# Kernel optimization log

Hardware: AMD Instinct MI355X
Metric: run time of the kernel (lower is better)

## Reference

```python
import jax, jax.numpy as jnp
import numpy as np

N_NODES = 40000
N_EDGES = 640000
IN_FEATS = 256
EDGE_FEATS = 64
OUT_FEATS = 128
NUM_HEADS = 8
D = OUT_FEATS // NUM_HEADS  # 16


def setup_inputs() -> dict:
    key = jax.random.key(0)
    ks = jax.random.split(key, 9)
    node_feats = jax.random.normal(ks[0], (N_NODES, IN_FEATS), dtype=jnp.float32)
    edge_feats = jax.random.normal(ks[1], (N_EDGES, EDGE_FEATS), dtype=jnp.float32)
    src = jax.random.randint(ks[2], (N_EDGES,), 0, N_NODES, dtype=jnp.int32)
    dst = jax.random.randint(ks[3], (N_EDGES,), 0, N_NODES, dtype=jnp.int32)
    # learned parameters (xavier-ish scale)
    node_w = jax.random.normal(ks[4], (OUT_FEATS, IN_FEATS), dtype=jnp.float32) * (2.0 / (IN_FEATS + OUT_FEATS)) ** 0.5
    node_b = jnp.zeros((OUT_FEATS,), dtype=jnp.float32)
    edge_w = jax.random.normal(ks[5], (OUT_FEATS, EDGE_FEATS), dtype=jnp.float32) * (2.0 / (EDGE_FEATS + OUT_FEATS)) ** 0.5
    edge_b = jnp.zeros((OUT_FEATS,), dtype=jnp.float32)
    attn = jax.random.normal(ks[6], (1, NUM_HEADS, 3 * D), dtype=jnp.float32) * 0.1
    return {"node_feats": node_feats, "edge_feats": edge_feats, "src": src, "dst": dst,
            "node_w": node_w, "node_b": node_b, "edge_w": edge_w, "edge_b": edge_b, "attn": attn}


def reference(node_feats, edge_feats, src, dst, node_w, node_b, edge_w, edge_b, attn):
    N = node_feats.shape[0]
    # Node / edge projections -> [N,H,D], [E,H,D]
    Wh = (node_feats @ node_w.T + node_b).reshape(-1, NUM_HEADS, D)
    We = (edge_feats @ edge_w.T + edge_b).reshape(-1, NUM_HEADS, D)
    # Split attn into src/dst/edge parts: attn is [1,H,3D]
    a = attn[0]  # [H,3D]
    a_src, a_dst, a_e = a[:, :D], a[:, D:2 * D], a[:, 2 * D:]
    # Per-node partial scores [N,H], then gather per edge; edge part [E,H]
    s_src = jnp.einsum('nhd,hd->nh', Wh, a_src)
    s_dst = jnp.einsum('nhd,hd->nh', Wh, a_dst)
    s_e = jnp.einsum('ehd,hd->eh', We, a_e)
    e = s_src[src] + s_dst[dst] + s_e  # [E,H]
    e = jax.nn.leaky_relu(e, negative_slope=0.2)
    # Edge softmax over incoming edges of each dst node
    m = jax.ops.segment_max(e, dst, num_segments=N)          # [N,H]
    ex = jnp.exp(e - m[dst])                                  # [E,H]
    z = jax.ops.segment_sum(ex, dst, num_segments=N)          # [N,H]
    alpha = ex / z[dst]                                       # [E,H]
    # Weighted scatter-sum aggregation of source features
    msg = alpha[:, :, None] * Wh[src]                         # [E,H,D]
    h = jax.ops.segment_sum(msg, dst, num_segments=N)         # [N,H,D]
    return h.reshape(N, NUM_HEADS * D)
```

## Files before the change

### kernel.cpp

```cpp
#include <hip/hip_runtime.h>
#include <hip/hip_fp16.h>
#include <stdint.h>
#include <stddef.h>

#define N_NODES   40000
#define N_EDGES   640000
#define IN_FEATS  256
#define EDGE_FEATS 64
#define OUT_FEATS 128
#define NUM_HEADS 8
#define HD        16

typedef __attribute__((ext_vector_type(8))) short  short8;
typedef __attribute__((ext_vector_type(4))) float  floatx4;

__device__ inline short f2bf(float f) {
  union { float f; uint32_t u; } v; v.f = f;
  uint32_t r = v.u + 0x7fffu + ((v.u >> 16) & 1u);
  return (short)(r >> 16);
}

__device__ inline short8 cvt8(float4 lo, float4 hi) {
  short8 r;
  r[0] = f2bf(lo.x); r[1] = f2bf(lo.y); r[2] = f2bf(lo.z); r[3] = f2bf(lo.w);
  r[4] = f2bf(hi.x); r[5] = f2bf(hi.y); r[6] = f2bf(hi.z); r[7] = f2bf(hi.w);
  return r;
}

__device__ inline float bflo(uint32_t w) {
  union { uint32_t u; float f; } v; v.u = w << 16; return v.f;
}
__device__ inline float bfhi(uint32_t w) {
  union { uint32_t u; float f; } v; v.u = w & 0xffff0000u; return v.f;
}

__global__ __launch_bounds__(512) void prep_hist_kernel(
    const float* __restrict__ edge_w, const float* __restrict__ edge_b,
    const float* __restrict__ attn, const float* __restrict__ node_w,
    const int* __restrict__ dst,
    float* __restrict__ Wfold, float* __restrict__ bfold,
    uint32_t* __restrict__ Wbf, int* __restrict__ deg) {
  int tid = threadIdx.x;
  if (blockIdx.x == 0) {
    int h = tid >> 6, k = tid & 63;
    float s = 0.f;
    #pragma unroll
    for (int d = 0; d < HD; d++)
      s += edge_w[(h * HD + d) * EDGE_FEATS + k] * attn[h * 48 + 32 + d];
    Wfold[h * EDGE_FEATS + k] = s;
    if (k == 0) {
      float b = 0.f;
      #pragma unroll
      for (int d = 0; d < HD; d++)
        b += edge_b[h * HD + d] * attn[h * 48 + 32 + d];
      bfold[h] = b;
    }
    const float2* W2 = (const float2*)node_w;
    #pragma unroll
    for (int j = 0; j < 32; j++) {
      int p = j * 512 + tid;
      float2 f = W2[p];
      Wbf[p] = (uint32_t)(uint16_t)f2bf(f.x) |
               ((uint32_t)(uint16_t)f2bf(f.y) << 16);
    }
  } else {
    int e = (blockIdx.x - 1) * 512 + tid;
    atomicAdd(&deg[dst[e]], 1);
  }
}

__global__ __launch_bounds__(256) void wh_gemm(
    const float* __restrict__ A,
    const uint32_t* __restrict__ Wbf,
    const float* __restrict__ bias,
    uint32_t* __restrict__ Whp) {
  int wave = (blockIdx.x * blockDim.x + threadIdx.x) >> 6;
  int lane = threadIdx.x & 63;
  int m0 = wave * 16;
  if (m0 >= N_NODES) return;
  int row = lane & 15, quad = lane >> 4;

  floatx4 acc[8];
  #pragma unroll
  for (int nt = 0; nt < 8; nt++) acc[nt] = (floatx4)(0.f);

  const float4* A4 = (const float4*)A;
  const uint4*  W4 = (const uint4*)Wbf;
  int a_base = ((m0 + row) * IN_FEATS + quad * 8) >> 2;

  #pragma unroll
  for (int s = 0; s < 8; s++) {
    float4 alo = A4[a_base + s * 8];
    float4 ahi = A4[a_base + s * 8 + 1];
    short8 af = cvt8(alo, ahi);
    #pragma unroll
    for (int nt = 0; nt < 8; nt++) {
      int fo = (nt * 16 + row) * IN_FEATS + s * 32 + quad * 8;
      uint4 u = W4[fo >> 3];
      short8 bf = *(short8*)&u;
      acc[nt] = __builtin_amdgcn_mfma_f32_16x16x32_bf16(af, bf, acc[nt], 0, 0, 0);
    }
  }
  #pragma unroll
  for (int nt = 0; nt < 4; nt++) {
    float blo_ = bias[nt * 16 + row];
    float bhi_ = bias[64 + nt * 16 + row];
    #pragma unroll
    for (int r = 0; r < 4; r++) {
      int m = m0 + quad * 4 + r;
      float lo = acc[nt][r] + blo_;
      float hi = acc[nt + 4][r] + bhi_;
      uint32_t d = (uint32_t)(uint16_t)f2bf(lo) |
                   ((uint32_t)(uint16_t)f2bf(hi) << 16);
      Whp[m * 64 + nt * 16 + row] = d;
    }
  }
}

__global__ __launch_bounds__(256) void ssd_kernel(
    const uint32_t* __restrict__ Whp, const float* __restrict__ attn,
    float* __restrict__ s_src, float* __restrict__ s_dst) {
  int t = blockIdx.x * 256 + threadIdx.x;
  int n = t >> 2, hp = t & 3;
  const uint4* p = (const uint4*)(Whp + n * 64 + hp * 16);
  const float* as_lo = attn + hp * 48;
  const float* ad_lo = attn + hp * 48 + 16;
  const float* as_hi = attn + (hp + 4) * 48;
  const float* ad_hi = attn + (hp + 4) * 48 + 16;
  float ss_lo = 0.f, sd_lo = 0.f, ss_hi = 0.f, sd_hi = 0.f;
  #pragma unroll
  for (int q = 0; q < 4; q++) {
    uint4 u = p[q];
    uint32_t ws[4] = {u.x, u.y, u.z, u.w};
    #pragma unroll
    for (int k = 0; k < 4; k++) {
      int d = q * 4 + k;
      float lo = bflo(ws[k]), hi = bfhi(ws[k]);
      ss_lo += lo * as_lo[d]; sd_lo += lo * ad_lo[d];
      ss_hi += hi * as_hi[d]; sd_hi += hi * ad_hi[d];
    }
  }
  s_src[n * 8 + hp]     = ss_lo;
  s_src[n * 8 + hp + 4] = ss_hi;
  s_dst[n * 8 + hp]     = sd_lo;
  s_dst[n * 8 + hp + 4] = sd_hi;
}

__global__ __launch_bounds__(1024) void scan_kernel(
    const int* __restrict__ deg, int* __restrict__ rs, int* __restrict__ cursor) {
  __shared__ int wsum[16];
  __shared__ int carry;
  int tid = threadIdx.x;
  int lane = tid & 63, w = tid >> 6;
  if (tid == 0) carry = 0;
  __syncthreads();
  for (int chunk = 0; chunk < 40; chunk++) {
    int i = chunk * 1024 + tid;
    int v = (i < N_NODES) ? deg[i] : 0;
    int x = v;
    #pragma unroll
    for (int off = 1; off < 64; off <<= 1) {
      int y = __shfl_up(x, off, 64);
      if (lane >= off) x += y;
    }
    if (lane == 63) wsum[w] = x;
    __syncthreads();
    int p = carry, tot = 0;
    #pragma unroll
    for (int j = 0; j < 16; j++) {
      int s = wsum[j];
      if (j < w) p += s;
      tot += s;
    }
    int excl = p + x - v;
    if (i < N_NODES) { rs[i] = excl; cursor[i] = excl; }
    __syncthreads();
    if (tid == 0) carry += tot;
  }
  __syncthreads();
  if (tid == 0) rs[N_NODES] = carry;
}

__global__ __launch_bounds__(256) void edge_kernel(
    const float* __restrict__ edge_feats, const int* __restrict__ src,
    const int* __restrict__ dst, const float* __restrict__ Wfold,
    const float* __restrict__ bfold, const float* __restrict__ s_src,
    const float* __restrict__ s_dst, uint4* __restrict__ lg16) {
  int e = blockIdx.x * 256 + threadIdx.x;
  int s = src[e], d = dst[e];
  const float4* ss4 = (const float4*)(s_src + (size_t)s * 8);
  const float4* sd4 = (const float4*)(s_dst + (size_t)d * 8);
  float4 sa = ss4[0], sb = ss4[1];
  float4 da = sd4[0], db = sd4[1];

  float acc[8];
  #pragma unroll
  for (int h = 0; h < 8; h++) acc[h] = bfold[h];
  const float4* ef4 = (const float4*)(edge_feats + (size_t)e * EDGE_FEATS);
  #pragma unroll
  for (int k4 = 0; k4 < 16; k4++) {
    float4 f = ef4[k4];
    #pragma unroll
    for (int h = 0; h < 8; h++) {
      const float* wr = Wfold + h * EDGE_FEATS + k4 * 4;
      acc[h] += f.x * wr[0] + f.y * wr[1] + f.z * wr[2] + f.w * wr[3];
    }
  }
  float v[8];
  v[0] = acc[0] + sa.x + da.x; v[1] = acc[1] + sa.y + da.y;
  v[2] = acc[2] + sa.z + da.z; v[3] = acc[3] + sa.w + da.w;
  v[4] = acc[4] + sb.x + db.x; v[5] = acc[5] + sb.y + db.y;
  v[6] = acc[6] + sb.z + db.z; v[7] = acc[7] + sb.w + db.w;
  #pragma unroll
  for (int h = 0; h < 8; h++) v[h] = v[h] > 0.f ? v[h] : 0.2f * v[h];

  uint32_t pk[4];
  #pragma unroll
  for (int j = 0; j < 4; j++) {
    uint32_t lo = __half_as_ushort(__float2half_rn(v[2 * j]));
    uint32_t hi = __half_as_ushort(__float2half_rn(v[2 * j + 1]));
    pk[j] = lo | (hi << 16);
  }
  lg16[e] = make_uint4(pk[0], pk[1], pk[2], pk[3]);
}

__global__ __launch_bounds__(256) void scatter_kernel(
    const int* __restrict__ src, const int* __restrict__ dst,
    int* __restrict__ cursor, int2* __restrict__ csr8) {
  int e = blockIdx.x * 256 + threadIdx.x;
  int d = dst[e];
  int s = src[e];
  int pos = atomicAdd(&cursor[d], 1);
  csr8[pos] = make_int2(e, s);
}

__global__ __launch_bounds__(256) void aggregate_kernel(
    const int* __restrict__ rs, const int2* __restrict__ csr8,
    const uint4* __restrict__ lg16, const uint32_t* __restrict__ Whp,
    float* __restrict__ out) {
  int node = blockIdx.x * 4 + (threadIdx.x >> 6);
  int lane = threadIdx.x & 63;
  int h1 = lane >> 4;
  int start = rs[node], end = rs[node + 1];
  uint32_t sh = (h1 & 1) * 16;
  bool hi_pair = (h1 & 2) != 0;

  float z1 = 0.f, z2 = 0.f, a1 = 0.f, a2 = 0.f;

  #define STEP(g, wv)                                                  \
    {                                                                  \
      uint32_t c1 = hi_pair ? (g).y : (g).x;                           \
      uint32_t c2 = hi_pair ? (g).w : (g).z;                           \
      float l1 = __half2float(__ushort_as_half((uint16_t)(c1 >> sh))); \
      float l2 = __half2float(__ushort_as_half((uint16_t)(c2 >> sh))); \
      float e1 = __expf(l1), e2 = __expf(l2);                          \
      z1 += e1; z2 += e2;                                              \
      a1 += e1 * bflo(wv); a2 += e2 * bfhi(wv);                        \
    }

  int i = start;
  for (; i + 3 < end; i += 4) {
    int2 r0 = csr8[i], r1 = csr8[i + 1], r2 = csr8[i + 2], r3 = csr8[i + 3];
    uint4 g0 = lg16[r0.x], g1 = lg16[r1.x], g2 = lg16[r2.x], g3 = lg16[r3.x];
    uint32_t w0 = Whp[(size_t)r0.y * 64 + lane];
    uint32_t w1 = Whp[(size_t)r1.y * 64 + lane];
    uint32_t w2 = Whp[(size_t)r2.y * 64 + lane];
    uint32_t w3 = Whp[(size_t)r3.y * 64 + lane];
    STEP(g0, w0); STEP(g1, w1); STEP(g2, w2); STEP(g3, w3);
  }
  for (; i < end; i++) {
    int2 r0 = csr8[i];
    uint4 g0 = lg16[r0.x];
    uint32_t w0 = Whp[(size_t)r0.y * 64 + lane];
    STEP(g0, w0);
  }
  #undef STEP

  float o1 = (end > start) ? a1 / z1 : 0.f;
  float o2 = (end > start) ? a2 / z2 : 0.f;
  out[(size_t)node * OUT_FEATS + lane] = o1;
  out[(size_t)node * OUT_FEATS + 64 + lane] = o2;
}

extern "C" void kernel_launch(void* const* d_in, const int* in_sizes, int n_in,
                              void* d_out, int out_size, void* d_ws, size_t ws_size,
                              hipStream_t stream) {
  const float* node_feats = (const float*)d_in[0];
  const float* edge_feats = (const float*)d_in[1];
  const int*   src        = (const int*)d_in[2];
  const int*   dst        = (const int*)d_in[3];
  const float* node_w     = (const float*)d_in[4];
  const float* node_b     = (const float*)d_in[5];
  const float* edge_w     = (const float*)d_in[6];
  const float* edge_b     = (const float*)d_in[7];
  const float* attn       = (const float*)d_in[8];
  float* out = (float*)d_out;

  char* ws = (char*)d_ws;
  size_t off = 0;
  auto alloc = [&](size_t bytes) {
    void* p = ws + off;
    off += (bytes + 255) & ~(size_t)255;
    return p;
  };
  uint32_t* Whp      = (uint32_t*)alloc((size_t)N_NODES * 64 * 4);
  float*    s_src    = (float*)alloc((size_t)N_NODES * NUM_HEADS * 4);
  float*    s_dst    = (float*)alloc((size_t)N_NODES * NUM_HEADS * 4);
  uint4*    lg16     = (uint4*)alloc((size_t)N_EDGES * 16);
  int2*     csr8     = (int2*)alloc((size_t)N_EDGES * 8);
  int*      deg      = (int*)alloc((size_t)N_NODES * 4);
  int*      rs       = (int*)alloc((size_t)(N_NODES + 1) * 4);
  int*      cursor   = (int*)alloc((size_t)N_NODES * 4);
  float*    Wfold    = (float*)alloc(NUM_HEADS * EDGE_FEATS * 4);
  float*    bfold    = (float*)alloc(NUM_HEADS * 4);
  uint32_t* Wbf      = (uint32_t*)alloc((size_t)OUT_FEATS * IN_FEATS * 2);

  hipMemsetAsync(deg, 0, (size_t)N_NODES * 4, stream);

  prep_hist_kernel<<<1 + N_EDGES / 512, 512, 0, stream>>>(
      edge_w, edge_b, attn, node_w, dst, Wfold, bfold, Wbf, deg);
  wh_gemm<<<N_NODES / 16 / 4, 256, 0, stream>>>(node_feats, Wbf, node_b, Whp);
  ssd_kernel<<<N_NODES * 4 / 256, 256, 0, stream>>>(Whp, attn, s_src, s_dst);
  scan_kernel<<<1, 1024, 0, stream>>>(deg, rs, cursor);
  edge_kernel<<<N_EDGES / 256, 256, 0, stream>>>(edge_feats, src, dst, Wfold,
                                                 bfold, s_src, s_dst, lg16);
  scatter_kernel<<<N_EDGES / 256, 256, 0, stream>>>(src, dst, cursor, csr8);
  aggregate_kernel<<<N_NODES / 4, 256, 0, stream>>>(rs, csr8, lg16, Whp, out);
}
```

Before: 471.9 us.

## Split each node's edges across two waves and halve scan iterations

```diff
diff --git a/kernel.cpp b/kernel.cpp
--- a/kernel.cpp
+++ b/kernel.cpp
@@ -154,9 +154,11 @@
   int lane = tid & 63, w = tid >> 6;
   if (tid == 0) carry = 0;
   __syncthreads();
-  for (int chunk = 0; chunk < 40; chunk++) {
-    int i = chunk * 1024 + tid;
-    int v = (i < N_NODES) ? deg[i] : 0;
+  const int2* deg2 = (const int2*)deg;
+  for (int chunk = 0; chunk < 20; chunk++) {
+    int i2 = chunk * 1024 + tid;
+    int2 dv = (i2 < N_NODES / 2) ? deg2[i2] : make_int2(0, 0);
+    int v = dv.x + dv.y;
     int x = v;
     #pragma unroll
     for (int off = 1; off < 64; off <<= 1) {
@@ -173,7 +175,10 @@
       tot += s;
     }
     int excl = p + x - v;
-    if (i < N_NODES) { rs[i] = excl; cursor[i] = excl; }
+    if (i2 < N_NODES / 2) {
+      rs[2 * i2]     = excl;      cursor[2 * i2]     = excl;
+      rs[2 * i2 + 1] = excl + dv.x; cursor[2 * i2 + 1] = excl + dv.x;
+    }
     __syncthreads();
     if (tid == 0) carry += tot;
   }
@@ -238,10 +243,18 @@
     const int* __restrict__ rs, const int2* __restrict__ csr8,
     const uint4* __restrict__ lg16, const uint32_t* __restrict__ Whp,
     float* __restrict__ out) {
-  int node = blockIdx.x * 4 + (threadIdx.x >> 6);
+  __shared__ float red[2][4][64];
+  int w = threadIdx.x >> 6;
   int lane = threadIdx.x & 63;
+  int nib = w >> 1;
+  int sub = w & 1;
+  int node = blockIdx.x * 2 + nib;
   int h1 = lane >> 4;
   int start = rs[node], end = rs[node + 1];
+  int cnt = end - start;
+  int half = (cnt + 1) >> 1;
+  int s0 = start + sub * half;
+  int e0 = min(end, s0 + half);
   uint32_t sh = (h1 & 1) * 16;
   bool hi_pair = (h1 & 2) != 0;
 
@@ -258,17 +271,32 @@
       a1 += e1 * bflo(wv); a2 += e2 * bfhi(wv);                        \
     }
 
-  int i = start;
-  for (; i + 3 < end; i += 4) {
-    int2 r0 = csr8[i], r1 = csr8[i + 1], r2 = csr8[i + 2], r3 = csr8[i + 3];
-    uint4 g0 = lg16[r0.x], g1 = lg16[r1.x], g2 = lg16[r2.x], g3 = lg16[r3.x];
-    uint32_t w0 = Whp[(size_t)r0.y * 64 + lane];
-    uint32_t w1 = Whp[(size_t)r1.y * 64 + lane];
-    uint32_t w2 = Whp[(size_t)r2.y * 64 + lane];
-    uint32_t w3 = Whp[(size_t)r3.y * 64 + lane];
-    STEP(g0, w0); STEP(g1, w1); STEP(g2, w2); STEP(g3, w3);
-  }
-  for (; i < end; i++) {
+  int i = s0;
+  for (; i + 7 < e0; i += 8) {
+    int2 r[8]; uint4 g[8]; uint32_t wv[8];
+    #pragma unroll
+    for (int j = 0; j < 8; j++) r[j] = csr8[i + j];
+    #pragma unroll
+    for (int j = 0; j < 8; j++) {
+      g[j] = lg16[r[j].x];
+      wv[j] = Whp[(size_t)r[j].y * 64 + lane];
+    }
+    #pragma unroll
+    for (int j = 0; j < 8; j++) STEP(g[j], wv[j]);
+  }
+  for (; i + 3 < e0; i += 4) {
+    int2 r[4]; uint4 g[4]; uint32_t wv[4];
+    #pragma unroll
+    for (int j = 0; j < 4; j++) r[j] = csr8[i + j];
+    #pragma unroll
+    for (int j = 0; j < 4; j++) {
+      g[j] = lg16[r[j].x];
+      wv[j] = Whp[(size_t)r[j].y * 64 + lane];
+    }
+    #pragma unroll
+    for (int j = 0; j < 4; j++) STEP(g[j], wv[j]);
+  }
+  for (; i < e0; i++) {
     int2 r0 = csr8[i];
     uint4 g0 = lg16[r0.x];
     uint32_t w0 = Whp[(size_t)r0.y * 64 + lane];
@@ -276,10 +304,19 @@
   }
   #undef STEP
 
-  float o1 = (end > start) ? a1 / z1 : 0.f;
-  float o2 = (end > start) ? a2 / z2 : 0.f;
-  out[(size_t)node * OUT_FEATS + lane] = o1;
-  out[(size_t)node * OUT_FEATS + 64 + lane] = o2;
+  if (sub == 1) {
+    red[nib][0][lane] = z1; red[nib][1][lane] = z2;
+    red[nib][2][lane] = a1; red[nib][3][lane] = a2;
+  }
+  __syncthreads();
+  if (sub == 0) {
+    z1 += red[nib][0][lane]; z2 += red[nib][1][lane];
+    a1 += red[nib][2][lane]; a2 += red[nib][3][lane];
+    float o1 = (cnt > 0) ? a1 / z1 : 0.f;
+    float o2 = (cnt > 0) ? a2 / z2 : 0.f;
+    out[(size_t)node * OUT_FEATS + lane] = o1;
+    out[(size_t)node * OUT_FEATS + 64 + lane] = o2;
+  }
 }
 
 extern "C" void kernel_launch(void* const* d_in, const int* in_sizes, int n_in,
@@ -325,5 +362,5 @@
   edge_kernel<<<N_EDGES / 256, 256, 0, stream>>>(edge_feats, src, dst, Wfold,
                                                  bfold, s_src, s_dst, lg16);
   scatter_kernel<<<N_EDGES / 256, 256, 0, stream>>>(src, dst, cursor, csr8);
-  aggregate_kernel<<<N_NODES / 4, 256, 0, stream>>>(rs, csr8, lg16, Whp, out);
-}
+  aggregate_kernel<<<N_NODES / 2, 256, 0, stream>>>(rs, csr8, lg16, Whp, out);
+}
```

Result: slower. 521.6 us (+10.5%).
